# Kernel tuning notes

Measured on AMD Instinct MI355X. Metric: run time of the kernel, lower is better.

## Reference

```python
import itertools
import jax, jax.numpy as jnp
import numpy as np

# ---- config (mirrors args) ----
BS = 8; C = 20              # 4 + num_sem_categories
FH, FW = 480, 640           # frame height/width
DU = 2                      # du_scale
NSC = 16                    # num_sem_categories
RES = 5; ZRES = 5           # xy / z map resolution (cm)
MAP_CM = 4800 // 2          # map_size_cm // global_downscaling
VR = 100                    # vision_range
HFOV = 79.0
MAXH = int(200 / ZRES); MINH = int(-40 / ZRES)   # 40, -8
AGENT_H = 0.88 * 100.0
CAT_T, EXP_T, MAP_T = 5.0, 1.0, 1.0
STAIR_R = 30
DEG = 57.29577951308232
M = MAP_CM // RES           # 480 local map cells

CAM_XC = (FW - 1.) / 2.
CAM_ZC = (FH - 1.) / 2.
CAM_F = (FW / 2.) / np.tan(np.deg2rad(HFOV / 2.))
SHIFT_X = VR * RES // 2     # shift_loc theta = pi/2 -> identity rotation, +x only

def _circle_mask(r):
    size = 2 * r
    ii, jj = np.meshgrid(np.arange(size), np.arange(size), indexing='ij')
    return (((ii + 0.5 - size // 2) ** 2 + (jj + 0.5 - size // 2) ** 2) <= r ** 2).astype(np.float32)

CIRCLE = jnp.asarray(_circle_mask(STAIR_R))

def splat_feat_nd(init_grid, feat, coords):
    # init_grid [B,F,d0,d1,d2], feat [B,F,N], coords [B,3,N] in [-1,1]
    B, nF = init_grid.shape[:2]
    gd = init_grid.shape[2:]
    grid_flat = init_grid.reshape(B, nF, -1)
    pos_dim, wts_dim = [], []
    for d in range(3):
        pos = coords[:, d, :] * gd[d] / 2 + gd[d] / 2
        pd, wd = [], []
        for ix in (0, 1):
            pos_ix = jnp.floor(pos) + ix
            safe = ((pos_ix > 0) & (pos_ix < gd[d])).astype(pos.dtype)
            wd.append((1 - jnp.abs(pos - pos_ix)) * safe)
            pd.append(pos_ix * safe)
        pos_dim.append(pd); wts_dim.append(wd)
    idxs, vals = [], []
    for ix_d in itertools.product((0, 1), repeat=3):  # 8 trilinear corners
        index = jnp.zeros_like(pos_dim[0][0])
        wts = jnp.ones_like(wts_dim[0][0])
        for d in range(3):
            index = index * gd[d] + pos_dim[d][ix_d[d]]
            wts = wts * wts_dim[d][ix_d[d]]
        idxs.append(index.astype(jnp.int32))
        vals.append(feat * wts[:, None, :])
    idx = jnp.concatenate(idxs, -1)          # [B, 8N]
    val = jnp.concatenate(vals, -1)          # [B, F, 8N]
    grid_flat = jax.vmap(lambda g, i, v: g.at[:, i].add(v))(grid_flat, idx, val)
    return jnp.round(grid_flat).reshape(init_grid.shape)

def affine_grid(theta, H, W):
    # F.affine_grid, align_corners=False (torch default)
    xs = (jnp.arange(W, dtype=theta.dtype) + 0.5) * 2 / W - 1
    ys = (jnp.arange(H, dtype=theta.dtype) + 0.5) * 2 / H - 1
    gy, gx = jnp.meshgrid(ys, xs, indexing='ij')
    base = jnp.stack([gx, gy, jnp.ones_like(gx)], -1)   # [H,W,3]
    return jnp.einsum('bij,hwj->bhwi', theta, base)     # [B,H,W,2]

def grid_sample(img, grid):
    # bilinear, zero padding, align_corners=True
    B, C_, H, W = img.shape
    gx = (grid[..., 0] + 1.) * (W - 1) / 2.
    gy = (grid[..., 1] + 1.) * (H - 1) / 2.
    x0 = jnp.floor(gx); y0 = jnp.floor(gy)
    def gather(ix, iy):
        valid = ((ix >= 0) & (ix < W) & (iy >= 0) & (iy < H)).astype(img.dtype)
        ic = jnp.clip(ix, 0, W - 1).astype(jnp.int32)
        jc = jnp.clip(iy, 0, H - 1).astype(jnp.int32)
        v = jax.vmap(lambda im, yy, xx: im[:, yy, xx])(img, jc, ic)  # [B,C,H,W]
        return v * valid[:, None]
    wx1 = gx - x0; wx0 = 1 - wx1; wy1 = gy - y0; wy0 = 1 - wy1
    return (gather(x0, y0) * (wx0 * wy0)[:, None]
            + gather(x0 + 1, y0) * (wx1 * wy0)[:, None]
            + gather(x0, y0 + 1) * (wx0 * wy1)[:, None]
            + gather(x0 + 1, y0 + 1) * (wx1 * wy1)[:, None])

def maxpool3(x):
    return jax.lax.reduce_window(x, -jnp.inf, jax.lax.max,
                                 (1, 1, 3, 3), (1, 1, 1, 1),
                                 [(0, 0), (0, 0), (1, 1), (1, 1)])

def _forward(obs, pose_obs, maps_last, poses_last, eve_angle):
    bs, c, h, w = obs.shape
    hs, ws = h // DU, w // DU
    depth = obs[:, 3, ::DU, ::DU]
    # point cloud from depth (du.get_point_cloud_from_z_t)
    xg = jnp.arange(0, w, DU, dtype=obs.dtype)[None, None, :]
    zg = (h - 1 - jnp.arange(0, h, DU, dtype=obs.dtype))[None, :, None]
    X = (xg - CAM_XC) * depth / CAM_F
    Z = (zg - CAM_ZC) * depth / CAM_F
    # camera elevation rotation about x-axis (per-env eve_angle) + sensor height
    th = jnp.deg2rad(eve_angle)[:, None, None]
    ct, st = jnp.cos(th), jnp.sin(th)
    Yr = ct * depth - st * Z
    Zr = st * depth + ct * Z + AGENT_H
    Xs = X + SHIFT_X
    # normalize to [-1,1] voxel coords
    cx = (Xs / RES - VR // 2) / VR * 2.0
    cy = (Yr / RES - VR // 2) / VR * 2.0
    cz = (Zr / ZRES - (MAXH + MINH) // 2) / (MAXH - MINH) * 2.0
    coords = jnp.stack([cx.reshape(bs, -1), cy.reshape(bs, -1), cz.reshape(bs, -1)], 1)
    sem = obs[:, 4:].reshape(bs, c - 4, hs, DU, ws, DU).mean((3, 5))  # AvgPool2d(du)
    feat = jnp.concatenate([jnp.ones((bs, 1, hs * ws), obs.dtype),
                            sem.reshape(bs, c - 4, hs * ws)], 1)
    init_grid = jnp.zeros((bs, 1 + NSC, VR, VR, MAXH - MINH), obs.dtype)
    voxels = splat_feat_nd(init_grid, feat, coords).transpose(0, 1, 3, 2, 4)
    min_z = int(25 / ZRES - MINH)
    max_z = int((AGENT_H + 50) / ZRES - MINH)
    mid_z = int(AGENT_H / ZRES - MINH)
    ah_proj = voxels[..., min_z:max_z].sum(-1)
    stair_proj = voxels[..., mid_z - 5:mid_z].sum(-1)
    all_proj = voxels.sum(-1)
    fp_map = jnp.clip(ah_proj[:, 0:1] / MAP_T, 0., 1.)
    fp_stair = jnp.clip(stair_proj[:, 0:1] / MAP_T, 0., 1.)
    fp_exp = jnp.clip(all_proj[:, 0:1] / EXP_T, 0., 1.)
    x1 = M // 2 - VR // 2; x2 = x1 + VR; y1 = M // 2; y2 = y1 + VR
    agent_view = jnp.zeros((bs, c, M, M), obs.dtype)
    agent_view = agent_view.at[:, 0:1, y1:y2, x1:x2].set(fp_map)
    agent_view = agent_view.at[:, 1:2, y1:y2, x1:x2].set(fp_exp)
    agent_view = agent_view.at[:, 4:, y1:y2, x1:x2].set(jnp.clip(ah_proj[:, 1:] / CAT_T, 0., 1.))
    agent_view_stair = jax.lax.stop_gradient(agent_view).at[:, 0:1, y1:y2, x1:x2].set(fp_stair)
    # pose integration (get_new_pose_batch)
    tr = poses_last[:, 2] / DEG
    ny = poses_last[:, 1] + pose_obs[:, 0] * jnp.sin(tr) + pose_obs[:, 1] * jnp.cos(tr)
    nx = poses_last[:, 0] + pose_obs[:, 0] * jnp.cos(tr) - pose_obs[:, 1] * jnp.sin(tr)
    no = poses_last[:, 2] + pose_obs[:, 2] * DEG
    no = jnp.fmod(no - 180.0, 360.0) + 180.0
    no = jnp.fmod(no + 180.0, 360.0) - 180.0
    current_poses = jnp.stack([nx, ny, no], 1)
    cp = jax.lax.stop_gradient(current_poses)  # st_pose = clone().detach()
    half = M // 2
    st_xy = -(cp[:, :2] * 100.0 / RES - half) / half
    st_t = (90.0 - cp[:, 2]) * np.pi / 180.0
    c_, s_ = jnp.cos(st_t), jnp.sin(st_t)
    zeros = jnp.zeros_like(c_); ones = jnp.ones_like(c_)
    theta1 = jnp.stack([jnp.stack([c_, -s_, zeros], 1), jnp.stack([s_, c_, zeros], 1)], 1)
    theta2 = jnp.stack([jnp.stack([ones, zeros, st_xy[:, 0]], 1),
                        jnp.stack([zeros, ones, st_xy[:, 1]], 1)], 1)
    rot_grid = affine_grid(theta1, M, M)
    trans_grid = affine_grid(theta2, M, M)
    translated = grid_sample(grid_sample(agent_view, rot_grid), trans_grid)
    diff = translated[:, 1:2] - maxpool3(translated[:, 0:1])
    diff = jnp.where(diff > 0.8, 1.0, 0.0).astype(obs.dtype)
    maps2 = jnp.maximum(maps_last, translated)
    m0 = (eve_angle == 0)[:, None, None, None] & (diff == 1.0)
    map_pred = maps2.at[:, 0:1].set(jnp.where(m0, 0.0, maps2[:, 0:1]))
    # stair map
    translated_stair = grid_sample(grid_sample(agent_view_stair, rot_grid), trans_grid)
    s_y = jnp.clip((cp[0, 1] * 100 / 5).astype(jnp.int32), STAIR_R, M - STAIR_R - 1)
    s_x = jnp.clip((cp[0, 0] * 100 / 5).astype(jnp.int32), STAIR_R, M - STAIR_R - 1)
    full_mask = jax.lax.dynamic_update_slice(jnp.zeros((M, M), obs.dtype), CIRCLE.astype(obs.dtype),
                                             (s_y - STAIR_R, s_x - STAIR_R))
    translated_stair = translated_stair.at[0, 0:2].multiply(full_mask)
    diff_s = translated_stair[:, 1:2] - translated_stair[:, 0:1]
    diff_s = jnp.where(diff_s > 0.8, 1.0, 0.0).astype(obs.dtype)
    maps3 = jnp.maximum(maps_last, translated_stair)
    m0s = (eve_angle == 0)[:, None, None, None] & (diff_s == 1.0)
    map_pred_stair = maps3.at[:, 0:1].set(jnp.where(m0s, 0.0, maps3[:, 0:1]))
    return translated, map_pred, map_pred_stair, current_poses

def setup_inputs() -> dict:
    key = jax.random.key(0)
    k1, k2, k3, k4, k5 = jax.random.split(key, 5)
    obs = jax.random.uniform(k1, (BS, C, FH, FW), jnp.float32)
    depth = 50.0 + 350.0 * jax.random.uniform(k2, (BS, FH, FW), jnp.float32)  # depth in cm
    obs = obs.at[:, 3].set(depth)
    pose_obs = jax.random.normal(k3, (BS, 3), jnp.float32) * jnp.array([0.1, 0.05, 0.02], jnp.float32)
    maps_last = jax.random.uniform(k4, (BS, C, M, M), jnp.float32)
    poses_last = (jnp.tile(jnp.array([12.0, 12.0, 0.0], jnp.float32), (BS, 1))
                  + jax.random.normal(k5, (BS, 3), jnp.float32) * jnp.array([0.5, 0.5, 30.0], jnp.float32))
    eve_angle = jnp.array([0., 0., -30., 0., 30., 0., 0., 0.], jnp.float32)
    return {'obs': obs, 'pose_obs': pose_obs, 'maps_last': maps_last,
            'poses_last': poses_last, 'eve_angle': eve_angle}

def reference(obs, pose_obs, maps_last, poses_last, eve_angle):
    return _forward(obs, pose_obs, maps_last, poses_last, eve_angle)
```

## Files before the change

### kernel.cpp

```cpp
#include <hip/hip_runtime.h>
#include <cmath>

#define NBS 8
#define NC 20
#define NFH 480
#define NFW 640
#define NHS 240
#define NWS 320
#define NM 480
#define NPIX (NM * NM)
#define NVR 100
#define NPIXELS (NBS * NHS * NWS)
#define PPB (NHS * NWS)

constexpr long long T_OFF    = 0LL;
constexpr long long P_OFF    = 36864000LL;
constexpr long long S_OFF    = 73728000LL;
constexpr long long POSE_OFF = 110592000LL;

constexpr long long SMAP_OFF = P_OFF;
constexpr long long PAR_OFF  = SMAP_OFF + 1520000LL;
constexpr long long TS_OFF   = PAR_OFF + 64LL;
constexpr long long POOL_OFF = TS_OFF + 1843200LL;
constexpr long long REC_OFF  = POOL_OFF + 9830400LL;
constexpr long long ENT_OFF  = REC_OFF + 9830400LL;
constexpr long long CNT_OFF  = ENT_OFF + 9830400LL;
constexpr long long OFF2_OFF = CNT_OFF + 80000LL;
constexpr long long CUR_OFF  = OFF2_OFF + 80000LL;

__device__ __forceinline__ float clamp01(float x) {
    return fminf(fmaxf(x, 0.0f), 1.0f);
}

__global__ void k_pose(const float* __restrict__ pose_obs,
                       const float* __restrict__ poses_last,
                       float* __restrict__ outp) {
    int b = threadIdx.x;
    if (b >= NBS) return;
    float* pose_out = outp + POSE_OFF;
    float* par = outp + PAR_OFF;
    const float DEGf = 57.29577951308232f;
    float tr = poses_last[b * 3 + 2] / DEGf;
    float s_tr = sinf(tr), c_tr = cosf(tr);
    float ny = poses_last[b * 3 + 1] + pose_obs[b * 3 + 0] * s_tr + pose_obs[b * 3 + 1] * c_tr;
    float nx = poses_last[b * 3 + 0] + pose_obs[b * 3 + 0] * c_tr - pose_obs[b * 3 + 1] * s_tr;
    float no = poses_last[b * 3 + 2] + pose_obs[b * 3 + 2] * DEGf;
    no = fmodf(no - 180.0f, 360.0f) + 180.0f;
    no = fmodf(no + 180.0f, 360.0f) - 180.0f;
    pose_out[b * 3 + 0] = nx;
    pose_out[b * 3 + 1] = ny;
    pose_out[b * 3 + 2] = no;
    float stx = -((nx * 100.0f) / 5.0f - 240.0f) / 240.0f;
    float sty = -((ny * 100.0f) / 5.0f - 240.0f) / 240.0f;
    float stt = ((90.0f - no) * 3.14159265358979323846f) / 180.0f;
    par[b * 4 + 0] = cosf(stt);
    par[b * 4 + 1] = sinf(stt);
    par[b * 4 + 2] = stx;
    par[b * 4 + 3] = sty;
    if (b == 0) {
        int sy = (int)((ny * 100.0f) / 5.0f);
        int sx = (int)((nx * 100.0f) / 5.0f);
        sy = min(max(sy, 30), NM - 31);
        sx = min(max(sx, 30), NM - 31);
        par[32] = (float)sy;
        par[33] = (float)sx;
    }
}

__global__ void k_count(const float* __restrict__ obs,
                        const float* __restrict__ eve, float camf,
                        unsigned int* __restrict__ counts,
                        float* __restrict__ pooled,
                        float4* __restrict__ rec) {
    int tid = blockIdx.x * blockDim.x + threadIdx.x;
    if (tid >= NPIXELS) return;
    int b = tid / PPB;
    int p = tid % PPB;
    int iy = p / NWS, ix = p % NWS;
    const float* ob = obs + (long long)b * NC * NFH * NFW;
    float depth = ob[(3LL * NFH + 2 * iy) * NFW + 2 * ix];
    float th = eve[b] * 0.017453292519943295f;
    float ct = cosf(th), st = sinf(th);
    float X = ((float)(2 * ix) - 319.5f) * depth / camf;
    float Z = ((float)(479 - 2 * iy) - 239.5f) * depth / camf;
    float Yr = ct * depth - st * Z;
    float Zr = st * depth + ct * Z + 88.0f;
    float Xs = X + 250.0f;
    float cx = ((Xs / 5.0f) - 50.0f) / 100.0f * 2.0f;
    float cy = ((Yr / 5.0f) - 50.0f) / 100.0f * 2.0f;
    float cz = ((Zr / 5.0f) - 16.0f) / 48.0f * 2.0f;
    float posx = (cx * 100.0f) / 2.0f + 50.0f;
    float posy = (cy * 100.0f) / 2.0f + 50.0f;
    float posz = (cz * 48.0f) / 2.0f + 24.0f;
    bool alive = (posx > 0.0f) && (posx < 100.0f) &&
                 (posy > 0.0f) && (posy < 100.0f) &&
                 (posz > 0.0f) && (posz < 48.0f);
    rec[tid] = make_float4(posx, posy, posz, alive ? 1.0f : 0.0f);
    if (!alive) return;
    int fx = (int)floorf(posx);
    int fy = (int)floorf(posy);
    atomicAdd(&counts[b * 10000 + fx * 100 + fy], 1u);
    if (posz > 12.0f && posz < 35.0f) {
        float sem[16];
#pragma unroll
        for (int k = 0; k < 16; ++k) {
            const float* q = ob + ((long long)(4 + k) * NFH + 2 * iy) * NFW + 2 * ix;
            sem[k] = (q[0] + q[1] + q[NFW] + q[NFW + 1]) * 0.25f;
        }
        float4* pp = (float4*)(pooled + (long long)tid * 16);
#pragma unroll
        for (int g = 0; g < 4; ++g)
            pp[g] = make_float4(sem[4 * g], sem[4 * g + 1], sem[4 * g + 2], sem[4 * g + 3]);
    }
}

__global__ void k_scan(const unsigned int* __restrict__ counts,
                       unsigned int* __restrict__ offs,
                       unsigned int* __restrict__ curs) {
    int b = blockIdx.x;
    int lane = threadIdx.x;
    unsigned int base = 0;
    for (int c0 = 0; c0 < 10000; c0 += 64) {
        int i = c0 + lane;
        unsigned int v = (i < 10000) ? counts[b * 10000 + i] : 0u;
        unsigned int s = v;
#pragma unroll
        for (int d = 1; d < 64; d <<= 1) {
            unsigned int t = __shfl_up(s, d);
            if (lane >= d) s += t;
        }
        if (i < 10000) {
            unsigned int excl = base + s - v;
            offs[b * 10000 + i] = excl;
            curs[b * 10000 + i] = excl;
        }
        base += __shfl(s, 63);
    }
}

__global__ void k_fill(const float4* __restrict__ rec,
                       unsigned int* __restrict__ curs,
                       float4* __restrict__ entries) {
    int tid = blockIdx.x * blockDim.x + threadIdx.x;
    if (tid >= NPIXELS) return;
    float4 r = rec[tid];
    if (r.w == 0.0f) return;
    int b = tid / PPB;
    int fx = (int)floorf(r.x);
    int fy = (int)floorf(r.y);
    unsigned int slot = atomicAdd(&curs[b * 10000 + fx * 100 + fy], 1u);
    entries[(long long)b * PPB + slot] =
        make_float4(r.x, r.y, r.z, __uint_as_float((unsigned int)tid));
}

__global__ void __launch_bounds__(64) k_accum(const float4* __restrict__ entries,
                                              const unsigned int* __restrict__ counts,
                                              const unsigned int* __restrict__ offs,
                                              const float* __restrict__ pooled,
                                              float* __restrict__ smap) {
    int col = blockIdx.x;
    int b = col / 10000;
    int xy = col % 10000;
    int x = xy / 100, y = xy % 100;
    __shared__ float acc[400];
    int lane = threadIdx.x;
    for (int i = lane; i < 400; i += 64) acc[i] = 0.0f;
    __syncthreads();
    if (x >= 1 && y >= 1) {
        const float4* eb = entries + (long long)b * PPB;
#pragma unroll
        for (int dbx = 0; dbx < 2; ++dbx) {
            int bx = x - 1 + dbx;
            if (bx > 99) continue;
#pragma unroll
            for (int dby = 0; dby < 2; ++dby) {
                int by = y - 1 + dby;
                if (by > 99) continue;
                int bucket = b * 10000 + bx * 100 + by;
                unsigned int n = counts[bucket];
                unsigned int s0 = offs[bucket];
                for (unsigned int e0 = 0; e0 < n; e0 += 64) {
                    unsigned int e = e0 + (unsigned int)lane;
                    if (e < n) {
                        float4 ent = eb[s0 + e];
                        float wx = 1.0f - fabsf(ent.x - (float)x);
                        float wy = 1.0f - fabsf(ent.y - (float)y);
                        float wxy = wx * wy;
                        if (wxy > 0.0f) {
                            float posz = ent.z;
                            float fz = floorf(posz);
#pragma unroll
                            for (int d = 0; d < 2; ++d) {
                                float zf = fz + (float)d;
                                int z = (int)zf;
                                if (z < 1 || z > 47) continue;
                                float w = wxy * (1.0f - fabsf(posz - zf));
                                if (w <= 0.0f) continue;
                                atomicAdd(&acc[z], w);
                                if (z >= 13 && z < 35) {
                                    const float* sp =
                                        pooled + (long long)__float_as_uint(ent.w) * 16;
                                    float* ap = &acc[48 + (z - 13) * 16];
#pragma unroll
                                    for (int k = 0; k < 16; ++k)
                                        atomicAdd(&ap[k], sp[k] * w);
                                }
                            }
                        }
                    }
                }
            }
        }
    }
    __syncthreads();
    for (int i = lane; i < 400; i += 64) acc[i] = rintf(acc[i]);
    __syncthreads();
    float* sm = smap + (long long)b * 19 * 10000;
    int ij = y * 100 + x;
    if (lane < 16) {
        float s = 0.0f;
#pragma unroll
        for (int z = 13; z < 35; ++z) s += acc[48 + (z - 13) * 16 + lane];
        sm[(3 + lane) * 10000 + ij] = clamp01(s / 5.0f);
    } else if (lane == 16) {
        float s = 0.0f;
        for (int z = 13; z < 35; ++z) s += acc[z];
        sm[ij] = clamp01(s);
    } else if (lane == 17) {
        float s = 0.0f;
        for (int z = 0; z < 48; ++z) s += acc[z];
        sm[10000 + ij] = clamp01(s);
    } else if (lane == 18) {
        float s = 0.0f;
        for (int z = 20; z < 25; ++z) s += acc[z];
        sm[20000 + ij] = clamp01(s);
    }
}

__global__ void k_translate(float* __restrict__ outp,
                            const float* __restrict__ smap,
                            const float* __restrict__ par,
                            float* __restrict__ tstair) {
    int tid = blockIdx.x * blockDim.x + threadIdx.x;
    if (tid >= NBS * NPIX) return;
    int b = tid / NPIX;
    int ij = tid % NPIX;
    int i = ij / NM, j = ij % NM;
    float c = par[b * 4 + 0], s = par[b * 4 + 1];
    float stx = par[b * 4 + 2], sty = par[b * 4 + 3];
    float gx = (((float)j + 0.5f) * 2.0f) / 480.0f - 1.0f;
    float gy = (((float)i + 0.5f) * 2.0f) / 480.0f - 1.0f;
    float px = ((gx + stx) + 1.0f) * 479.0f / 2.0f;
    float py = ((gy + sty) + 1.0f) * 479.0f / 2.0f;
    float x0 = floorf(px), y0 = floorf(py);
    float wx1 = px - x0, wx0 = 1.0f - wx1;
    float wy1 = py - y0, wy0 = 1.0f - wy1;
    int offs[16];
    float wts[16];
    int nt = 0;
#pragma unroll
    for (int t = 0; t < 4; ++t) {
        int ox = t & 1, oy = t >> 1;
        float xo = x0 + (float)ox, yo = y0 + (float)oy;
        if (!(xo >= 0.0f && xo < 480.0f && yo >= 0.0f && yo < 480.0f)) continue;
        float wo = (ox ? wx1 : wx0) * (oy ? wy1 : wy0);
        int ixo = (int)xo, iyo = (int)yo;
        float gx2 = (((float)ixo + 0.5f) * 2.0f) / 480.0f - 1.0f;
        float gy2 = (((float)iyo + 0.5f) * 2.0f) / 480.0f - 1.0f;
        float rx = c * gx2 - s * gy2;
        float ry = s * gx2 + c * gy2;
        float qx = (rx + 1.0f) * 479.0f / 2.0f;
        float qy = (ry + 1.0f) * 479.0f / 2.0f;
        float xq0 = floorf(qx), yq0 = floorf(qy);
        float u1 = qx - xq0, u0 = 1.0f - u1;
        float v1 = qy - yq0, v0 = 1.0f - v1;
#pragma unroll
        for (int t2 = 0; t2 < 4; ++t2) {
            int ax = t2 & 1, ay = t2 >> 1;
            float xa = xq0 + (float)ax, ya = yq0 + (float)ay;
            if (xa >= 190.0f && xa < 290.0f && ya >= 240.0f && ya < 340.0f) {
                float w = wo * ((ax ? u1 : u0) * (ay ? v1 : v0));
                if (w != 0.0f) {
                    offs[nt] = ((int)ya - 240) * 100 + ((int)xa - 190);
                    wts[nt] = w;
                    ++nt;
                }
            }
        }
    }
    float* To = outp + T_OFF;
    long long obase = (long long)b * NC * NPIX + ij;
    if (nt == 0) {
#pragma unroll
        for (int ch = 0; ch < NC; ++ch) To[obase + (long long)ch * NPIX] = 0.0f;
        tstair[(long long)b * NPIX + ij] = 0.0f;
        return;
    }
    const float* sm = smap + (long long)b * 19 * 10000;
    float a0 = 0.0f, a1 = 0.0f, as_ = 0.0f;
    float cat[16];
#pragma unroll
    for (int k = 0; k < 16; ++k) cat[k] = 0.0f;
    for (int t = 0; t < nt; ++t) {
        float w = wts[t];
        int o = offs[t];
        a0 += w * sm[o];
        a1 += w * sm[10000 + o];
        as_ += w * sm[20000 + o];
#pragma unroll
        for (int k = 0; k < 16; ++k) cat[k] += w * sm[(3 + k) * 10000 + o];
    }
    To[obase] = a0;
    To[obase + (long long)NPIX] = a1;
    To[obase + 2LL * NPIX] = 0.0f;
    To[obase + 3LL * NPIX] = 0.0f;
#pragma unroll
    for (int k = 0; k < 16; ++k) To[obase + (long long)(4 + k) * NPIX] = cat[k];
    tstair[(long long)b * NPIX + ij] = as_;
}

__global__ void k_stair(const float* __restrict__ T, const float* __restrict__ tstair,
                        const float* __restrict__ par, const float* __restrict__ maps_last,
                        const float* __restrict__ eve, float* __restrict__ outS) {
    int tid = blockIdx.x * blockDim.x + threadIdx.x;
    if (tid >= NBS * NPIX) return;
    int b = tid / NPIX;
    int ij = tid % NPIX;
    int i = ij / NM, j = ij % NM;
    bool eve0 = (eve[b] == 0.0f);
    const float* Tb = T + (long long)b * NC * NPIX;
    float ts0 = tstair[(long long)b * NPIX + ij];
    float t1 = Tb[(long long)NPIX + ij];
    if (b == 0) {
        float dy = (float)i - par[32] + 0.5f;
        float dx = (float)j - par[33] + 0.5f;
        float mask = (dy * dy + dx * dx <= 900.0f) ? 1.0f : 0.0f;
        ts0 *= mask;
        t1 *= mask;
    }
    bool flag = (t1 - ts0) > 0.8f;
    const float* ml = maps_last + (long long)b * NC * NPIX;
    long long obase = (long long)b * NC * NPIX + ij;
#pragma unroll
    for (int ch = 0; ch < NC; ++ch) {
        float tch = (ch == 0) ? ts0 : (ch == 1) ? t1 : Tb[(long long)ch * NPIX + ij];
        float m3 = fmaxf(ml[(long long)ch * NPIX + ij], tch);
        outS[obase + (long long)ch * NPIX] = (ch == 0 && eve0 && flag) ? 0.0f : m3;
    }
}

__global__ void k_pred(const float* __restrict__ T, const float* __restrict__ maps_last,
                       const float* __restrict__ eve, float* __restrict__ outP) {
    int tid = blockIdx.x * blockDim.x + threadIdx.x;
    if (tid >= NBS * NPIX) return;
    int b = tid / NPIX;
    int ij = tid % NPIX;
    int i = ij / NM, j = ij % NM;
    const float* Tb = T + (long long)b * NC * NPIX;
    float mp = -INFINITY;
#pragma unroll
    for (int di = -1; di <= 1; ++di) {
        int ii = i + di;
        if (ii < 0 || ii >= NM) continue;
#pragma unroll
        for (int dj = -1; dj <= 1; ++dj) {
            int jj = j + dj;
            if (jj < 0 || jj >= NM) continue;
            mp = fmaxf(mp, Tb[(long long)ii * NM + jj]);
        }
    }
    float t1 = Tb[(long long)NPIX + ij];
    bool flag = (t1 - mp) > 0.8f;
    bool eve0 = (eve[b] == 0.0f);
    const float* ml = maps_last + (long long)b * NC * NPIX;
    long long obase = (long long)b * NC * NPIX + ij;
#pragma unroll
    for (int ch = 0; ch < NC; ++ch) {
        float m2 = fmaxf(ml[(long long)ch * NPIX + ij], Tb[(long long)ch * NPIX + ij]);
        outP[obase + (long long)ch * NPIX] = (ch == 0 && eve0 && flag) ? 0.0f : m2;
    }
}

extern "C" void kernel_launch(void* const* d_in, const int* in_sizes, int n_in,
                              void* d_out, int out_size, void* d_ws, size_t ws_size,
                              hipStream_t stream) {
    const float* obs = (const float*)d_in[0];
    const float* pose_obs = (const float*)d_in[1];
    const float* maps_last = (const float*)d_in[2];
    const float* poses_last = (const float*)d_in[3];
    const float* eve = (const float*)d_in[4];
    float* outp = (float*)d_out;

    float camf = (float)(320.0 / tan(39.5 * M_PI / 180.0));

    unsigned int* counts = (unsigned int*)(outp + CNT_OFF);
    unsigned int* offs2  = (unsigned int*)(outp + OFF2_OFF);
    unsigned int* curs   = (unsigned int*)(outp + CUR_OFF);
    float*  pooled  = outp + POOL_OFF;
    float4* rec     = (float4*)(outp + REC_OFF);
    float4* entries = (float4*)(outp + ENT_OFF);

    hipMemsetAsync(counts, 0, 80000 * sizeof(unsigned int), stream);

    k_pose<<<1, 64, 0, stream>>>(pose_obs, poses_last, outp);

    k_count<<<NPIXELS / 256, 256, 0, stream>>>(obs, eve, camf, counts, pooled, rec);

    k_scan<<<NBS, 64, 0, stream>>>(counts, offs2, curs);

    k_fill<<<NPIXELS / 256, 256, 0, stream>>>(rec, curs, entries);

    k_accum<<<NBS * 10000, 64, 0, stream>>>(entries, counts, offs2, pooled,
                                            outp + SMAP_OFF);

    k_translate<<<(NBS * NPIX) / 256, 256, 0, stream>>>(outp, outp + SMAP_OFF,
                                                        outp + PAR_OFF, outp + TS_OFF);

    k_stair<<<(NBS * NPIX) / 256, 256, 0, stream>>>(outp + T_OFF, outp + TS_OFF,
                                                    outp + PAR_OFF, maps_last, eve,
                                                    outp + S_OFF);

    k_pred<<<(NBS * NPIX) / 256, 256, 0, stream>>>(outp + T_OFF, maps_last, eve,
                                                   outp + P_OFF);
}
```

Before: 1.216 ms.

## Tile splat accumulation into 6x6 column blocks with inline semantic entries

Replaces the per-column accumulation (one 64-thread block per map column, four buckets read per column) with 6x6 column tiles. Each tile streams its contiguous bucket ranges once and accumulates into a large shared-memory buffer. Pooled semantic features now move from the count pass into the fill pass and are stored inline in 20-float entries, so the separate pooled buffer and its indirect gather are gone. The scan becomes a single 1024-thread block per batch instead of a serial 64-lane loop. The cost is about 58KB of LDS per block, which lowers occupancy, plus more shared atomics per block.

```diff
diff --git a/kernel.cpp b/kernel.cpp
--- a/kernel.cpp
+++ b/kernel.cpp
@@ -12,6 +12,10 @@
 #define NVR 100
 #define NPIXELS (NBS * NHS * NWS)
 #define PPB (NHS * NWS)
+#define ESTRIDE 20
+#define TILE 6
+#define NTILE 17
+#define CSTR 401
 
 constexpr long long T_OFF    = 0LL;
 constexpr long long P_OFF    = 36864000LL;
@@ -21,15 +25,38 @@
 constexpr long long SMAP_OFF = P_OFF;
 constexpr long long PAR_OFF  = SMAP_OFF + 1520000LL;
 constexpr long long TS_OFF   = PAR_OFF + 64LL;
-constexpr long long POOL_OFF = TS_OFF + 1843200LL;
-constexpr long long REC_OFF  = POOL_OFF + 9830400LL;
-constexpr long long ENT_OFF  = REC_OFF + 9830400LL;
-constexpr long long CNT_OFF  = ENT_OFF + 9830400LL;
+constexpr long long REC_OFF  = TS_OFF + 1843200LL;
+constexpr long long ENT_OFF  = REC_OFF + 2457600LL;
+constexpr long long CNT_OFF  = ENT_OFF + 12288000LL;
 constexpr long long OFF2_OFF = CNT_OFF + 80000LL;
 constexpr long long CUR_OFF  = OFF2_OFF + 80000LL;
 
 __device__ __forceinline__ float clamp01(float x) {
     return fminf(fmaxf(x, 0.0f), 1.0f);
+}
+
+__device__ __forceinline__ void project_px(const float* __restrict__ ob, float ev,
+                                           float camf, int iy, int ix,
+                                           float& posx, float& posy, float& posz,
+                                           bool& alive, bool& semz) {
+    float depth = ob[(3LL * NFH + 2 * iy) * NFW + 2 * ix];
+    float th = ev * 0.017453292519943295f;
+    float ct = cosf(th), st = sinf(th);
+    float X = ((float)(2 * ix) - 319.5f) * depth / camf;
+    float Z = ((float)(479 - 2 * iy) - 239.5f) * depth / camf;
+    float Yr = ct * depth - st * Z;
+    float Zr = st * depth + ct * Z + 88.0f;
+    float Xs = X + 250.0f;
+    float cx = ((Xs / 5.0f) - 50.0f) / 100.0f * 2.0f;
+    float cy = ((Yr / 5.0f) - 50.0f) / 100.0f * 2.0f;
+    float cz = ((Zr / 5.0f) - 16.0f) / 48.0f * 2.0f;
+    posx = (cx * 100.0f) / 2.0f + 50.0f;
+    posy = (cy * 100.0f) / 2.0f + 50.0f;
+    posz = (cz * 48.0f) / 2.0f + 24.0f;
+    alive = (posx > 0.0f) && (posx < 100.0f) &&
+            (posy > 0.0f) && (posy < 100.0f) &&
+            (posz > 0.0f) && (posz < 48.0f);
+    semz = (posz > 12.0f) && (posz < 35.0f);
 }
 
 __global__ void k_pose(const float* __restrict__ pose_obs,
@@ -70,7 +97,6 @@
 __global__ void k_count(const float* __restrict__ obs,
                         const float* __restrict__ eve, float camf,
                         unsigned int* __restrict__ counts,
-                        float* __restrict__ pooled,
                         float4* __restrict__ rec) {
     int tid = blockIdx.x * blockDim.x + threadIdx.x;
     if (tid >= NPIXELS) return;
@@ -78,162 +104,204 @@
     int p = tid % PPB;
     int iy = p / NWS, ix = p % NWS;
     const float* ob = obs + (long long)b * NC * NFH * NFW;
-    float depth = ob[(3LL * NFH + 2 * iy) * NFW + 2 * ix];
-    float th = eve[b] * 0.017453292519943295f;
-    float ct = cosf(th), st = sinf(th);
-    float X = ((float)(2 * ix) - 319.5f) * depth / camf;
-    float Z = ((float)(479 - 2 * iy) - 239.5f) * depth / camf;
-    float Yr = ct * depth - st * Z;
-    float Zr = st * depth + ct * Z + 88.0f;
-    float Xs = X + 250.0f;
-    float cx = ((Xs / 5.0f) - 50.0f) / 100.0f * 2.0f;
-    float cy = ((Yr / 5.0f) - 50.0f) / 100.0f * 2.0f;
-    float cz = ((Zr / 5.0f) - 16.0f) / 48.0f * 2.0f;
-    float posx = (cx * 100.0f) / 2.0f + 50.0f;
-    float posy = (cy * 100.0f) / 2.0f + 50.0f;
-    float posz = (cz * 48.0f) / 2.0f + 24.0f;
-    bool alive = (posx > 0.0f) && (posx < 100.0f) &&
-                 (posy > 0.0f) && (posy < 100.0f) &&
-                 (posz > 0.0f) && (posz < 48.0f);
-    rec[tid] = make_float4(posx, posy, posz, alive ? 1.0f : 0.0f);
+    float posx, posy, posz;
+    bool alive, semz;
+    project_px(ob, eve[b], camf, iy, ix, posx, posy, posz, alive, semz);
+    float flag = alive ? (semz ? 2.0f : 1.0f) : 0.0f;
+    rec[tid] = make_float4(posx, posy, posz, flag);
     if (!alive) return;
     int fx = (int)floorf(posx);
     int fy = (int)floorf(posy);
     atomicAdd(&counts[b * 10000 + fx * 100 + fy], 1u);
-    if (posz > 12.0f && posz < 35.0f) {
-        float sem[16];
-#pragma unroll
-        for (int k = 0; k < 16; ++k) {
-            const float* q = ob + ((long long)(4 + k) * NFH + 2 * iy) * NFW + 2 * ix;
-            sem[k] = (q[0] + q[1] + q[NFW] + q[NFW + 1]) * 0.25f;
-        }
-        float4* pp = (float4*)(pooled + (long long)tid * 16);
-#pragma unroll
-        for (int g = 0; g < 4; ++g)
-            pp[g] = make_float4(sem[4 * g], sem[4 * g + 1], sem[4 * g + 2], sem[4 * g + 3]);
-    }
-}
-
-__global__ void k_scan(const unsigned int* __restrict__ counts,
-                       unsigned int* __restrict__ offs,
-                       unsigned int* __restrict__ curs) {
+}
+
+__global__ void __launch_bounds__(1024) k_scan(const unsigned int* __restrict__ counts,
+                                               unsigned int* __restrict__ offs,
+                                               unsigned int* __restrict__ curs) {
     int b = blockIdx.x;
-    int lane = threadIdx.x;
-    unsigned int base = 0;
-    for (int c0 = 0; c0 < 10000; c0 += 64) {
-        int i = c0 + lane;
-        unsigned int v = (i < 10000) ? counts[b * 10000 + i] : 0u;
-        unsigned int s = v;
-#pragma unroll
-        for (int d = 1; d < 64; d <<= 1) {
-            unsigned int t = __shfl_up(s, d);
-            if (lane >= d) s += t;
-        }
-        if (i < 10000) {
-            unsigned int excl = base + s - v;
-            offs[b * 10000 + i] = excl;
-            curs[b * 10000 + i] = excl;
-        }
-        base += __shfl(s, 63);
-    }
-}
-
-__global__ void k_fill(const float4* __restrict__ rec,
+    int t = threadIdx.x;
+    int lane = t & 63, wid = t >> 6;
+    const unsigned int* cb = counts + b * 10000;
+    unsigned int base_i = (unsigned int)t * 10u;
+    unsigned int v[10];
+    unsigned int s = 0;
+#pragma unroll
+    for (int k = 0; k < 10; ++k) {
+        unsigned int i = base_i + (unsigned int)k;
+        unsigned int x = (i < 10000u) ? cb[i] : 0u;
+        v[k] = s;
+        s += x;
+    }
+    unsigned int incl = s;
+#pragma unroll
+    for (int d = 1; d < 64; d <<= 1) {
+        unsigned int u = __shfl_up(incl, d);
+        if (lane >= d) incl += u;
+    }
+    __shared__ unsigned int wtot[16];
+    __shared__ unsigned int wexc[16];
+    if (lane == 63) wtot[wid] = incl;
+    __syncthreads();
+    if (t == 0) {
+        unsigned int a = 0;
+        for (int i = 0; i < 16; ++i) { wexc[i] = a; a += wtot[i]; }
+    }
+    __syncthreads();
+    unsigned int tbase = wexc[wid] + (incl - s);
+#pragma unroll
+    for (int k = 0; k < 10; ++k) {
+        unsigned int i = base_i + (unsigned int)k;
+        if (i < 10000u) {
+            unsigned int e = tbase + v[k];
+            offs[b * 10000 + i] = e;
+            curs[b * 10000 + i] = e;
+        }
+    }
+}
+
+__global__ void k_fill(const float* __restrict__ obs,
+                       const float4* __restrict__ rec,
                        unsigned int* __restrict__ curs,
-                       float4* __restrict__ entries) {
+                       float* __restrict__ entries) {
     int tid = blockIdx.x * blockDim.x + threadIdx.x;
     if (tid >= NPIXELS) return;
     float4 r = rec[tid];
     if (r.w == 0.0f) return;
     int b = tid / PPB;
+    int p = tid % PPB;
+    int iy = p / NWS, ix = p % NWS;
     int fx = (int)floorf(r.x);
     int fy = (int)floorf(r.y);
     unsigned int slot = atomicAdd(&curs[b * 10000 + fx * 100 + fy], 1u);
-    entries[(long long)b * PPB + slot] =
-        make_float4(r.x, r.y, r.z, __uint_as_float((unsigned int)tid));
-}
-
-__global__ void __launch_bounds__(64) k_accum(const float4* __restrict__ entries,
-                                              const unsigned int* __restrict__ counts,
-                                              const unsigned int* __restrict__ offs,
-                                              const float* __restrict__ pooled,
-                                              float* __restrict__ smap) {
-    int col = blockIdx.x;
-    int b = col / 10000;
-    int xy = col % 10000;
-    int x = xy / 100, y = xy % 100;
-    __shared__ float acc[400];
-    int lane = threadIdx.x;
-    for (int i = lane; i < 400; i += 64) acc[i] = 0.0f;
+    float4 sem4[4];
+#pragma unroll
+    for (int g = 0; g < 4; ++g) sem4[g] = make_float4(0.f, 0.f, 0.f, 0.f);
+    if (r.w == 2.0f) {
+        const float* ob = obs + (long long)b * NC * NFH * NFW;
+        float sem[16];
+#pragma unroll
+        for (int k = 0; k < 16; ++k) {
+            const float* q = ob + ((long long)(4 + k) * NFH + 2 * iy) * NFW + 2 * ix;
+            sem[k] = (q[0] + q[1] + q[NFW] + q[NFW + 1]) * 0.25f;
+        }
+#pragma unroll
+        for (int g = 0; g < 4; ++g)
+            sem4[g] = make_float4(sem[4 * g], sem[4 * g + 1], sem[4 * g + 2], sem[4 * g + 3]);
+    }
+    float4* ep = (float4*)(entries + ((long long)b * PPB + slot) * ESTRIDE);
+    ep[0] = make_float4(r.x, r.y, r.z, 0.f);
+#pragma unroll
+    for (int g = 0; g < 4; ++g) ep[1 + g] = sem4[g];
+}
+
+__global__ void __launch_bounds__(256) k_accum(const float* __restrict__ entries,
+                                               const unsigned int* __restrict__ counts,
+                                               const unsigned int* __restrict__ offs,
+                                               float* __restrict__ smap) {
+    int tileId = blockIdx.x;
+    int b = tileId / (NTILE * NTILE);
+    int txy = tileId % (NTILE * NTILE);
+    int tx = txy / NTILE, ty = txy % NTILE;
+    int x0 = tx * TILE, y0 = ty * TILE;
+    int nx = min(TILE, 100 - x0), ny = min(TILE, 100 - y0);
+    int ncols = nx * ny;
+    __shared__ float acc[TILE * TILE * CSTR];
+    __shared__ unsigned int rstart[8];
+    __shared__ unsigned int rcum[9];
+    int tid = threadIdx.x;
+    for (int i = tid; i < ncols * CSTR; i += 256) acc[i] = 0.0f;
+    int bxLo = max(x0 - 1, 0), bxHi = min(x0 + nx - 1, 99);
+    int byLo = max(y0 - 1, 0), byHi = min(y0 + ny - 1, 99);
+    int nbx = bxHi - bxLo + 1;
+    if (tid < nbx) {
+        int bx = bxLo + tid;
+        unsigned int s = offs[b * 10000 + bx * 100 + byLo];
+        unsigned int e = offs[b * 10000 + bx * 100 + byHi] + counts[b * 10000 + bx * 100 + byHi];
+        rstart[tid] = s;
+        rcum[tid + 1] = e - s;
+    }
+    if (tid == 0) rcum[0] = 0;
     __syncthreads();
-    if (x >= 1 && y >= 1) {
-        const float4* eb = entries + (long long)b * PPB;
-#pragma unroll
-        for (int dbx = 0; dbx < 2; ++dbx) {
-            int bx = x - 1 + dbx;
-            if (bx > 99) continue;
-#pragma unroll
-            for (int dby = 0; dby < 2; ++dby) {
-                int by = y - 1 + dby;
-                if (by > 99) continue;
-                int bucket = b * 10000 + bx * 100 + by;
-                unsigned int n = counts[bucket];
-                unsigned int s0 = offs[bucket];
-                for (unsigned int e0 = 0; e0 < n; e0 += 64) {
-                    unsigned int e = e0 + (unsigned int)lane;
-                    if (e < n) {
-                        float4 ent = eb[s0 + e];
-                        float wx = 1.0f - fabsf(ent.x - (float)x);
-                        float wy = 1.0f - fabsf(ent.y - (float)y);
-                        float wxy = wx * wy;
-                        if (wxy > 0.0f) {
-                            float posz = ent.z;
-                            float fz = floorf(posz);
-#pragma unroll
-                            for (int d = 0; d < 2; ++d) {
-                                float zf = fz + (float)d;
-                                int z = (int)zf;
-                                if (z < 1 || z > 47) continue;
-                                float w = wxy * (1.0f - fabsf(posz - zf));
-                                if (w <= 0.0f) continue;
-                                atomicAdd(&acc[z], w);
-                                if (z >= 13 && z < 35) {
-                                    const float* sp =
-                                        pooled + (long long)__float_as_uint(ent.w) * 16;
-                                    float* ap = &acc[48 + (z - 13) * 16];
-#pragma unroll
-                                    for (int k = 0; k < 16; ++k)
-                                        atomicAdd(&ap[k], sp[k] * w);
-                                }
-                            }
-                        }
+    if (tid == 0)
+        for (int i = 0; i < nbx; ++i) rcum[i + 1] += rcum[i];
+    __syncthreads();
+    unsigned int E = rcum[nbx];
+    const float* eb = entries + (long long)b * PPB * ESTRIDE;
+    int cxMin = max(x0, 1), cyMin = max(y0, 1);
+    for (unsigned int t = tid; t < E; t += 256) {
+        int r = 0;
+        while (t >= rcum[r + 1]) ++r;
+        const float* ep = eb + (long long)(rstart[r] + (t - rcum[r])) * ESTRIDE;
+        float4 e0 = ((const float4*)ep)[0];
+        float posx = e0.x, posy = e0.y, posz = e0.z;
+        float fz = floorf(posz);
+        bool zsem = (posz > 12.0f) && (posz < 35.0f);
+        float4 s4[4];
+        if (zsem) {
+#pragma unroll
+            for (int g = 0; g < 4; ++g) s4[g] = ((const float4*)ep)[1 + g];
+        }
+        float sem[16];
+        if (zsem) {
+#pragma unroll
+            for (int g = 0; g < 4; ++g) {
+                sem[4 * g + 0] = s4[g].x; sem[4 * g + 1] = s4[g].y;
+                sem[4 * g + 2] = s4[g].z; sem[4 * g + 3] = s4[g].w;
+            }
+        }
+        int fxi = (int)floorf(posx), fyi = (int)floorf(posy);
+#pragma unroll
+        for (int a = 0; a < 2; ++a) {
+            int cx = fxi + a;
+            if (cx < cxMin || cx >= x0 + nx) continue;
+            float wx = 1.0f - fabsf(posx - (float)cx);
+#pragma unroll
+            for (int c2 = 0; c2 < 2; ++c2) {
+                int cy = fyi + c2;
+                if (cy < cyMin || cy >= y0 + ny) continue;
+                float wxy = wx * (1.0f - fabsf(posy - (float)cy));
+                if (wxy <= 0.0f) continue;
+                float* colp = acc + ((cx - x0) * ny + (cy - y0)) * CSTR;
+#pragma unroll
+                for (int d = 0; d < 2; ++d) {
+                    float zf = fz + (float)d;
+                    int z = (int)zf;
+                    if (z < 1 || z > 47) continue;
+                    float w = wxy * (1.0f - fabsf(posz - zf));
+                    if (w == 0.0f) continue;
+                    atomicAdd(colp + z, w);
+                    if (z >= 13 && z < 35) {
+                        float* ap = colp + 48 + (z - 13) * 16;
+#pragma unroll
+                        for (int k = 0; k < 16; ++k)
+                            atomicAdd(ap + k, sem[k] * w);
                     }
                 }
             }
         }
     }
     __syncthreads();
-    for (int i = lane; i < 400; i += 64) acc[i] = rintf(acc[i]);
-    __syncthreads();
-    float* sm = smap + (long long)b * 19 * 10000;
-    int ij = y * 100 + x;
-    if (lane < 16) {
+    float* smb = smap + (long long)b * 19 * 10000;
+    for (int o = tid; o < ncols * 19; o += 256) {
+        int lc = o / 19, ch = o % 19;
+        int cx = x0 + lc / ny, cy = y0 + lc % ny;
+        const float* colp = acc + lc * CSTR;
         float s = 0.0f;
-#pragma unroll
-        for (int z = 13; z < 35; ++z) s += acc[48 + (z - 13) * 16 + lane];
-        sm[(3 + lane) * 10000 + ij] = clamp01(s / 5.0f);
-    } else if (lane == 16) {
-        float s = 0.0f;
-        for (int z = 13; z < 35; ++z) s += acc[z];
-        sm[ij] = clamp01(s);
-    } else if (lane == 17) {
-        float s = 0.0f;
-        for (int z = 0; z < 48; ++z) s += acc[z];
-        sm[10000 + ij] = clamp01(s);
-    } else if (lane == 18) {
-        float s = 0.0f;
-        for (int z = 20; z < 25; ++z) s += acc[z];
-        sm[20000 + ij] = clamp01(s);
+        if (ch == 0) {
+            for (int z = 13; z < 35; ++z) s += rintf(colp[z]);
+            s = clamp01(s);
+        } else if (ch == 1) {
+            for (int z = 0; z < 48; ++z) s += rintf(colp[z]);
+            s = clamp01(s);
+        } else if (ch == 2) {
+            for (int z = 20; z < 25; ++z) s += rintf(colp[z]);
+            s = clamp01(s);
+        } else {
+            int k = ch - 3;
+            for (int z = 13; z < 35; ++z) s += rintf(colp[48 + (z - 13) * 16 + k]);
+            s = clamp01(s / 5.0f);
+        }
+        smb[ch * 10000 + cy * 100 + cx] = s;
     }
 }
 
@@ -396,22 +464,21 @@
     unsigned int* counts = (unsigned int*)(outp + CNT_OFF);
     unsigned int* offs2  = (unsigned int*)(outp + OFF2_OFF);
     unsigned int* curs   = (unsigned int*)(outp + CUR_OFF);
-    float*  pooled  = outp + POOL_OFF;
     float4* rec     = (float4*)(outp + REC_OFF);
-    float4* entries = (float4*)(outp + ENT_OFF);
+    float*  entries = outp + ENT_OFF;
 
     hipMemsetAsync(counts, 0, 80000 * sizeof(unsigned int), stream);
 
     k_pose<<<1, 64, 0, stream>>>(pose_obs, poses_last, outp);
 
-    k_count<<<NPIXELS / 256, 256, 0, stream>>>(obs, eve, camf, counts, pooled, rec);
-
-    k_scan<<<NBS, 64, 0, stream>>>(counts, offs2, curs);
-
-    k_fill<<<NPIXELS / 256, 256, 0, stream>>>(rec, curs, entries);
-
-    k_accum<<<NBS * 10000, 64, 0, stream>>>(entries, counts, offs2, pooled,
-                                            outp + SMAP_OFF);
+    k_count<<<NPIXELS / 256, 256, 0, stream>>>(obs, eve, camf, counts, rec);
+
+    k_scan<<<NBS, 1024, 0, stream>>>(counts, offs2, curs);
+
+    k_fill<<<NPIXELS / 256, 256, 0, stream>>>(obs, rec, curs, entries);
+
+    k_accum<<<NBS * NTILE * NTILE, 256, 0, stream>>>(entries, counts, offs2,
+                                                     outp + SMAP_OFF);
 
     k_translate<<<(NBS * NPIX) / 256, 256, 0, stream>>>(outp, outp + SMAP_OFF,
                                                         outp + PAR_OFF, outp + TS_OFF);
```

New measurement: 1.478 ms. 1.22x slower.
